# Performance work log

Measured on AMD Instinct MI355X. Metric: run time of the kernel, lower is better.

## Reference

```python
import jax, jax.numpy as jnp
import numpy as np

N = 100000   # nodes
E = 1600000  # edges
IN, H, C = 128, 128, 40


def setup_inputs() -> dict:
    key = jax.random.key(0)
    ks = jax.random.split(key, 8)
    feat = jax.random.normal(ks[0], (N, IN), jnp.float32)
    src = jax.random.randint(ks[1], (E,), 0, N, jnp.int32)
    dst = jax.random.randint(ks[2], (E,), 0, N, jnp.int32)
    # Glorot-ish init like dgl GraphConv.reset_parameters
    W0 = jax.random.normal(ks[3], (IN, H), jnp.float32) * (1.0 / np.sqrt(IN))
    W1 = jax.random.normal(ks[4], (H, H), jnp.float32) * (1.0 / np.sqrt(H))
    W2 = jax.random.normal(ks[5], (H, C), jnp.float32) * (1.0 / np.sqrt(H))
    b0 = jnp.zeros((H,), jnp.float32)
    b1 = jnp.zeros((H,), jnp.float32)
    b2 = jnp.zeros((C,), jnp.float32)
    return {"feat": feat, "src": src, "dst": dst,
            "W0": W0, "b0": b0, "W1": W1, "b1": b1, "W2": W2, "b2": b2}


def _graph_conv(h, src, dst, W, b):
    # dgl GraphConv with norm='both': D_out^{-1/2} pre-scale, sum-aggregate,
    # D_in^{-1/2} post-scale; degrees clamped to min 1. Weight applied before
    # aggregation (in_feats >= out_feats path) -- math is identical either way.
    ones = jnp.ones((src.shape[0],), h.dtype)
    deg_out = jnp.maximum(jax.ops.segment_sum(ones, src, num_segments=N), 1.0)
    deg_in = jnp.maximum(jax.ops.segment_sum(ones, dst, num_segments=N), 1.0)
    h = h * (deg_out ** -0.5)[:, None]
    h = h @ W                                   # [N, out]
    agg = jax.ops.segment_sum(h[src], dst, num_segments=N)  # gather+scatter
    return agg * (deg_in ** -0.5)[:, None] + b


def reference(feat, src, dst, W0, b0, W1, b1, W2, b2):
    h = jax.nn.relu(_graph_conv(feat, src, dst, W0, b0))  # dropout p=0 -> identity
    h = jax.nn.relu(_graph_conv(h, src, dst, W1, b1))
    return _graph_conv(h, src, dst, W2, b2)
```

## Files before the change

### kernel.cpp

```cpp
#include <hip/hip_runtime.h>

#define NN 100000
#define EE 1600000
#define ELLW 64
#define NXCD 8
#define RNG ((NN + NXCD - 1) / NXCD)
#define GEMMN ((NN + 31) / 32)
#define BUILDN ((EE / 256) * NXCD)

__device__ __forceinline__ unsigned int pack_bf2(float a, float b) {
    unsigned int ua = __float_as_uint(a);
    ua += 0x7FFFu + ((ua >> 16) & 1u);
    unsigned int ub = __float_as_uint(b);
    ub += 0x7FFFu + ((ub >> 16) & 1u);
    return (ua >> 16) | (ub & 0xFFFF0000u);
}

__device__ __forceinline__ void nt_store_f2(float* p, float x, float y) {
    unsigned long long v = (unsigned long long)__float_as_uint(x) |
                           ((unsigned long long)__float_as_uint(y) << 32);
    __builtin_nontemporal_store(v, (unsigned long long*)p);
}

__device__ __forceinline__ void gemm128_body(const float* __restrict__ X, const int* __restrict__ dout,
                                             const float* __restrict__ W, unsigned int* __restrict__ Y,
                                             int n, int row0, int tid, float* Xs, int scaled) {
    const float4* X4 = (const float4*)X;
#pragma unroll
    for (int idx = tid; idx < 1024; idx += 256) {
        int r = idx & 31, c4 = idx >> 5;
        int row = row0 + r;
        float4 v = make_float4(0.f, 0.f, 0.f, 0.f);
        float s = 0.f;
        if (row < n) {
            v = X4[(size_t)row * 32 + c4];
            s = scaled ? rsqrtf((float)max(1, dout[row])) : 1.f;
        }
        Xs[(c4 * 4 + 0) * 32 + r] = v.x * s;
        Xs[(c4 * 4 + 1) * 32 + r] = v.y * s;
        Xs[(c4 * 4 + 2) * 32 + r] = v.z * s;
        Xs[(c4 * 4 + 3) * 32 + r] = v.w * s;
    }
    __syncthreads();
    int cg = tid & 31;
    int rg = tid >> 5;
    float a[4][4];
#pragma unroll
    for (int r = 0; r < 4; ++r)
#pragma unroll
        for (int c = 0; c < 4; ++c) a[r][c] = 0.f;
    const float4* W4 = (const float4*)W;
#pragma unroll 4
    for (int k = 0; k < 128; ++k) {
        float4 xv = *(const float4*)&Xs[k * 32 + rg * 4];
        float4 wv = W4[k * 32 + cg];
        float xr[4] = {xv.x, xv.y, xv.z, xv.w};
        float wc[4] = {wv.x, wv.y, wv.z, wv.w};
#pragma unroll
        for (int r = 0; r < 4; ++r)
#pragma unroll
            for (int c = 0; c < 4; ++c) a[r][c] = fmaf(xr[r], wc[c], a[r][c]);
    }
    int rbase = row0 + rg * 4;
    uint2* Y2 = (uint2*)Y;
#pragma unroll
    for (int r = 0; r < 4; ++r) {
        if (rbase + r < n) {
            Y2[(size_t)(rbase + r) * 32 + cg] =
                make_uint2(pack_bf2(a[r][0], a[r][1]), pack_bf2(a[r][2], a[r][3]));
        }
    }
}

__global__ __launch_bounds__(256) void k_build_gemm0(const int* __restrict__ src, const int* __restrict__ dst,
                                                     int* __restrict__ din, int* __restrict__ dout,
                                                     int* __restrict__ ell,
                                                     const float* __restrict__ X, const float* __restrict__ W,
                                                     unsigned int* __restrict__ Y) {
    __shared__ float Xs[128 * 32];
    int tid = threadIdx.x;
    int q = blockIdx.x / 17, rem = blockIdx.x % 17;
    if (rem == 16) {
        gemm128_body(X, nullptr, W, Y, NN, q * 32, tid, Xs, 0);
        return;
    }
    int idx = q * 16 + rem;
    int r = idx & (NXCD - 1);
    int slice = idx >> 3;
    int i = slice * 256 + tid;
    if (i >= EE) return;
    int s = __builtin_nontemporal_load(&src[i]);
    int d = __builtin_nontemporal_load(&dst[i]);
    int lo = r * RNG, hi = lo + RNG;
    if (d >= lo && d < hi) {
        int p = atomicAdd(&din[d], 1);
        if (p < ELLW) ell[(size_t)d * ELLW + p] = s;
    }
    if (s >= lo && s < hi) {
        atomicAdd(&dout[s], 1);
    }
}

__global__ __launch_bounds__(256) void k_gemm128(const float* __restrict__ X, const int* __restrict__ dout,
                                                 const float* __restrict__ W, unsigned int* __restrict__ Y, int n) {
    __shared__ float Xs[128 * 32];
    gemm128_body(X, dout, W, Y, n, blockIdx.x * 32, threadIdx.x, Xs, 1);
}

__global__ __launch_bounds__(320) void k_gemm40(const float* __restrict__ X, const int* __restrict__ dout,
                                                const float* __restrict__ W, unsigned int* __restrict__ Y, int n) {
    __shared__ float Xs[128 * 64];
    int tid = threadIdx.x;
    int row0 = blockIdx.x * 64;
    const float4* X4 = (const float4*)X;
    for (int idx = tid; idx < 2048; idx += 320) {
        int r = idx & 63, c4 = idx >> 6;
        int row = row0 + r;
        float4 v = make_float4(0.f, 0.f, 0.f, 0.f);
        float s = 0.f;
        if (row < n) { v = X4[(size_t)row * 32 + c4]; s = rsqrtf((float)max(1, dout[row])); }
        Xs[(c4 * 4 + 0) * 64 + r] = v.x * s;
        Xs[(c4 * 4 + 1) * 64 + r] = v.y * s;
        Xs[(c4 * 4 + 2) * 64 + r] = v.z * s;
        Xs[(c4 * 4 + 3) * 64 + r] = v.w * s;
    }
    __syncthreads();
    int cg = tid % 20;
    int rg = tid / 20;
    float a0x=0,a0y=0, a1x=0,a1y=0, a2x=0,a2y=0, a3x=0,a3y=0;
    const float2* W2 = (const float2*)W;
#pragma unroll 4
    for (int k = 0; k < 128; ++k) {
        float4 xv = *(const float4*)&Xs[k * 64 + rg * 4];
        float2 wv = W2[k * 20 + cg];
        a0x += xv.x * wv.x; a0y += xv.x * wv.y;
        a1x += xv.y * wv.x; a1y += xv.y * wv.y;
        a2x += xv.z * wv.x; a2y += xv.z * wv.y;
        a3x += xv.w * wv.x; a3y += xv.w * wv.y;
    }
    int rbase = row0 + rg * 4;
    if (rbase + 0 < n) Y[(size_t)(rbase + 0) * 32 + cg] = pack_bf2(a0x, a0y);
    if (rbase + 1 < n) Y[(size_t)(rbase + 1) * 32 + cg] = pack_bf2(a1x, a1y);
    if (rbase + 2 < n) Y[(size_t)(rbase + 2) * 32 + cg] = pack_bf2(a2x, a2y);
    if (rbase + 3 < n) Y[(size_t)(rbase + 3) * 32 + cg] = pack_bf2(a3x, a3y);
}

__global__ __launch_bounds__(256) void k_gather128(const unsigned int* __restrict__ h, const int* __restrict__ din,
                                                   const int* __restrict__ dout, const int* __restrict__ ell,
                                                   const float* __restrict__ b, float* __restrict__ out,
                                                   int n, int do_relu, int so_mode) {
    int wv = threadIdx.x >> 6, lane = threadIdx.x & 63;
    int v = blockIdx.x * 4 + wv;
    if (v >= n) return;
    int dv = din[v];
    int cnt = min(dv, ELLW);
    int cl = ell[(size_t)v * ELLW + lane];
    int cls = (lane < cnt) ? cl : 0;
    float scl = 1.f;
    if (so_mode) scl = rsqrtf((float)max(1, dout[cls]));
    float sx = 0.f, sy = 0.f;
    for (int j = 0; j < cnt; j += 8) {
        int cc[8]; float mk[8]; unsigned int t[8];
#pragma unroll
        for (int k = 0; k < 8; ++k) {
            int jj = j + k;
            int jc = jj < cnt ? jj : cnt - 1;
            cc[k] = __shfl(cls, jc);
            float sw = __shfl(scl, jc);
            mk[k] = (jj < cnt) ? sw : 0.f;
        }
#pragma unroll
        for (int k = 0; k < 8; ++k)
            t[k] = h[(size_t)cc[k] * 64 + lane];
#pragma unroll
        for (int k = 0; k < 8; ++k) {
            float x = __uint_as_float(t[k] << 16);
            float y = __uint_as_float(t[k] & 0xFFFF0000u);
            sx = fmaf(mk[k], x, sx);
            sy = fmaf(mk[k], y, sy);
        }
    }
    float sc = rsqrtf((float)max(1, dv));
    float2 bb = ((const float2*)b)[lane];
    float ox = sx * sc + bb.x;
    float oy = sy * sc + bb.y;
    if (do_relu) { ox = fmaxf(ox, 0.f); oy = fmaxf(oy, 0.f); }
    nt_store_f2((float*)((float2*)out + (size_t)v * 64 + lane), ox, oy);
}

__global__ __launch_bounds__(256) void k_gather40(const unsigned short* __restrict__ h, const int* __restrict__ din,
                                                  const int* __restrict__ ell,
                                                  const float* __restrict__ b, float* __restrict__ out, int n) {
    int wv = threadIdx.x >> 6, lane = threadIdx.x & 63;
    int v = blockIdx.x * 4 + wv;
    if (v >= n) return;
    int dv = din[v];
    int cnt = min(dv, ELLW);
    int cl = ell[(size_t)v * ELLW + lane];
    int cls = (lane < cnt) ? cl : 0;
    float s = 0.f;
    for (int j = 0; j < cnt; j += 8) {
        int cc[8]; float mk[8]; unsigned short t[8];
#pragma unroll
        for (int k = 0; k < 8; ++k) {
            int jj = j + k;
            cc[k] = __shfl(cls, jj < cnt ? jj : cnt - 1);
            mk[k] = (jj < cnt) ? 1.f : 0.f;
        }
        if (lane < 40) {
#pragma unroll
            for (int k = 0; k < 8; ++k) t[k] = h[(size_t)cc[k] * 64 + lane];
#pragma unroll
            for (int k = 0; k < 8; ++k)
                s = fmaf(mk[k], __uint_as_float((unsigned int)t[k] << 16), s);
        }
    }
    if (lane < 40) {
        out[(size_t)v * 40 + lane] = s * rsqrtf((float)max(1, dv)) + b[lane];
    }
}

extern "C" void kernel_launch(void* const* d_in, const int* in_sizes, int n_in,
                              void* d_out, int out_size, void* d_ws, size_t ws_size,
                              hipStream_t stream) {
    const float* feat = (const float*)d_in[0];
    const int*   src  = (const int*)d_in[1];
    const int*   dst  = (const int*)d_in[2];
    const float* W0   = (const float*)d_in[3];
    const float* b0   = (const float*)d_in[4];
    const float* W1   = (const float*)d_in[5];
    const float* b1   = (const float*)d_in[6];
    const float* W2   = (const float*)d_in[7];
    const float* b2   = (const float*)d_in[8];
    float* out = (float*)d_out;

    char* w = (char*)d_ws;
    int*   din       = (int*)w;    w += (size_t)NN * 4;
    int*   dout      = (int*)w;    w += (size_t)NN * 4;
    int*   ell       = (int*)w;    w += (size_t)NN * ELLW * 4;
    unsigned int* h2 = (unsigned int*)w; w += (size_t)NN * 128 * 2;
    unsigned int* h40 = (unsigned int*)w; w += (size_t)NN * 32 * 4;
    float* agg       = (float*)w;  w += (size_t)NN * 128 * 4;

    hipMemsetAsync(d_ws, 0, (size_t)NN * 8, stream);

    int gath_grid = (NN + 3) / 4;

    k_build_gemm0<<<GEMMN * 17, 256, 0, stream>>>(src, dst, din, dout, ell, feat, W0, h2);
    k_gather128<<<gath_grid, 256, 0, stream>>>(h2, din, dout, ell, b0, agg, NN, 1, 1);
    k_gemm128<<<GEMMN, 256, 0, stream>>>(agg, dout, W1, h2, NN);
    k_gather128<<<gath_grid, 256, 0, stream>>>(h2, din, dout, ell, b1, agg, NN, 1, 0);
    k_gemm40<<<(NN + 63) / 64, 320, 0, stream>>>(agg, dout, W2, h40, NN);
    k_gather40<<<gath_grid, 256, 0, stream>>>((const unsigned short*)h40, din, ell, b2, out, NN);
}
```

Measured before the change: 567.0 us.

## Phase-partition gather by source-id range for L2 locality; unfuse build and first GEMM

Replaces the one-node-per-wave 128-wide gather with a kernel where each wave owns 13 destination nodes. It walks 13 phases, and in each phase gathers only neighbours whose source id falls in one 8192-node range (selected by ballot), so the rows being read from the bf16 feature table are meant to stay resident in L2. The first layer's out-degree pre-scale moves from the gather into the GEMM, which now runs as a separate kernel after a standalone graph-build kernel instead of being fused with it. In exchange, gathers are issued one neighbour at a time instead of 8-wide batches, which weakens memory-level parallelism. Splitting the fused build/GEMM launch also gives up the overlap between the atomic-heavy build and the GEMM.

```diff
diff --git a/kernel.cpp b/kernel.cpp
--- a/kernel.cpp
+++ b/kernel.cpp
@@ -7,6 +7,9 @@
 #define RNG ((NN + NXCD - 1) / NXCD)
 #define GEMMN ((NN + 31) / 32)
 #define BUILDN ((EE / 256) * NXCD)
+#define GBLK 2048
+#define NPW 13
+#define NPH 13
 
 __device__ __forceinline__ unsigned int pack_bf2(float a, float b) {
     unsigned int ua = __float_as_uint(a);
@@ -22,9 +25,30 @@
     __builtin_nontemporal_store(v, (unsigned long long*)p);
 }
 
-__device__ __forceinline__ void gemm128_body(const float* __restrict__ X, const int* __restrict__ dout,
-                                             const float* __restrict__ W, unsigned int* __restrict__ Y,
-                                             int n, int row0, int tid, float* Xs, int scaled) {
+__global__ __launch_bounds__(256) void k_build(const int* __restrict__ src, const int* __restrict__ dst,
+                                               int* __restrict__ din, int* __restrict__ dout,
+                                               int* __restrict__ ell, int e) {
+    int r = blockIdx.x & (NXCD - 1);
+    int slice = blockIdx.x >> 3;
+    int i = slice * 256 + threadIdx.x;
+    if (i >= e) return;
+    int s = __builtin_nontemporal_load(&src[i]);
+    int d = __builtin_nontemporal_load(&dst[i]);
+    int lo = r * RNG, hi = lo + RNG;
+    if (d >= lo && d < hi) {
+        int p = atomicAdd(&din[d], 1);
+        if (p < ELLW) ell[(size_t)d * ELLW + p] = s;
+    }
+    if (s >= lo && s < hi) {
+        atomicAdd(&dout[s], 1);
+    }
+}
+
+__global__ __launch_bounds__(256) void k_gemm128(const float* __restrict__ X, const int* __restrict__ deg,
+                                                 const float* __restrict__ W, unsigned int* __restrict__ Y, int n) {
+    __shared__ float Xs[128 * 32];
+    int tid = threadIdx.x;
+    int row0 = blockIdx.x * 32;
     const float4* X4 = (const float4*)X;
 #pragma unroll
     for (int idx = tid; idx < 1024; idx += 256) {
@@ -34,7 +58,7 @@
         float s = 0.f;
         if (row < n) {
             v = X4[(size_t)row * 32 + c4];
-            s = scaled ? rsqrtf((float)max(1, dout[row])) : 1.f;
+            s = rsqrtf((float)max(1, deg[row]));
         }
         Xs[(c4 * 4 + 0) * 32 + r] = v.x * s;
         Xs[(c4 * 4 + 1) * 32 + r] = v.y * s;
@@ -72,42 +96,7 @@
     }
 }
 
-__global__ __launch_bounds__(256) void k_build_gemm0(const int* __restrict__ src, const int* __restrict__ dst,
-                                                     int* __restrict__ din, int* __restrict__ dout,
-                                                     int* __restrict__ ell,
-                                                     const float* __restrict__ X, const float* __restrict__ W,
-                                                     unsigned int* __restrict__ Y) {
-    __shared__ float Xs[128 * 32];
-    int tid = threadIdx.x;
-    int q = blockIdx.x / 17, rem = blockIdx.x % 17;
-    if (rem == 16) {
-        gemm128_body(X, nullptr, W, Y, NN, q * 32, tid, Xs, 0);
-        return;
-    }
-    int idx = q * 16 + rem;
-    int r = idx & (NXCD - 1);
-    int slice = idx >> 3;
-    int i = slice * 256 + tid;
-    if (i >= EE) return;
-    int s = __builtin_nontemporal_load(&src[i]);
-    int d = __builtin_nontemporal_load(&dst[i]);
-    int lo = r * RNG, hi = lo + RNG;
-    if (d >= lo && d < hi) {
-        int p = atomicAdd(&din[d], 1);
-        if (p < ELLW) ell[(size_t)d * ELLW + p] = s;
-    }
-    if (s >= lo && s < hi) {
-        atomicAdd(&dout[s], 1);
-    }
-}
-
-__global__ __launch_bounds__(256) void k_gemm128(const float* __restrict__ X, const int* __restrict__ dout,
-                                                 const float* __restrict__ W, unsigned int* __restrict__ Y, int n) {
-    __shared__ float Xs[128 * 32];
-    gemm128_body(X, dout, W, Y, n, blockIdx.x * 32, threadIdx.x, Xs, 1);
-}
-
-__global__ __launch_bounds__(320) void k_gemm40(const float* __restrict__ X, const int* __restrict__ dout,
+__global__ __launch_bounds__(320) void k_gemm40(const float* __restrict__ X, const int* __restrict__ deg,
                                                 const float* __restrict__ W, unsigned int* __restrict__ Y, int n) {
     __shared__ float Xs[128 * 64];
     int tid = threadIdx.x;
@@ -118,7 +107,7 @@
         int row = row0 + r;
         float4 v = make_float4(0.f, 0.f, 0.f, 0.f);
         float s = 0.f;
-        if (row < n) { v = X4[(size_t)row * 32 + c4]; s = rsqrtf((float)max(1, dout[row])); }
+        if (row < n) { v = X4[(size_t)row * 32 + c4]; s = rsqrtf((float)max(1, deg[row])); }
         Xs[(c4 * 4 + 0) * 64 + r] = v.x * s;
         Xs[(c4 * 4 + 1) * 64 + r] = v.y * s;
         Xs[(c4 * 4 + 2) * 64 + r] = v.z * s;
@@ -145,47 +134,53 @@
     if (rbase + 3 < n) Y[(size_t)(rbase + 3) * 32 + cg] = pack_bf2(a3x, a3y);
 }
 
-__global__ __launch_bounds__(256) void k_gather128(const unsigned int* __restrict__ h, const int* __restrict__ din,
-                                                   const int* __restrict__ dout, const int* __restrict__ ell,
-                                                   const float* __restrict__ b, float* __restrict__ out,
-                                                   int n, int do_relu, int so_mode) {
-    int wv = threadIdx.x >> 6, lane = threadIdx.x & 63;
-    int v = blockIdx.x * 4 + wv;
-    if (v >= n) return;
-    int dv = din[v];
-    int cnt = min(dv, ELLW);
-    int cl = ell[(size_t)v * ELLW + lane];
-    int cls = (lane < cnt) ? cl : 0;
-    float scl = 1.f;
-    if (so_mode) scl = rsqrtf((float)max(1, dout[cls]));
-    float sx = 0.f, sy = 0.f;
-    for (int j = 0; j < cnt; j += 8) {
-        int cc[8]; float mk[8]; unsigned int t[8];
-#pragma unroll
-        for (int k = 0; k < 8; ++k) {
-            int jj = j + k;
-            int jc = jj < cnt ? jj : cnt - 1;
-            cc[k] = __shfl(cls, jc);
-            float sw = __shfl(scl, jc);
-            mk[k] = (jj < cnt) ? sw : 0.f;
-        }
-#pragma unroll
-        for (int k = 0; k < 8; ++k)
-            t[k] = h[(size_t)cc[k] * 64 + lane];
-#pragma unroll
-        for (int k = 0; k < 8; ++k) {
-            float x = __uint_as_float(t[k] << 16);
-            float y = __uint_as_float(t[k] & 0xFFFF0000u);
-            sx = fmaf(mk[k], x, sx);
-            sy = fmaf(mk[k], y, sy);
-        }
-    }
-    float sc = rsqrtf((float)max(1, dv));
+__global__ __launch_bounds__(256) void k_gather128p(const unsigned int* __restrict__ h,
+                                                    const int* __restrict__ din, const int* __restrict__ ell,
+                                                    const float* __restrict__ b, float* __restrict__ out,
+                                                    int do_relu) {
+    int lane = threadIdx.x & 63;
+    int gw = (blockIdx.x * 256 + threadIdx.x) >> 6;
+    int v0 = gw * NPW;
+    float sx[NPW], sy[NPW];
+    int cls[NPW];
+    int cnt[NPW];
+#pragma unroll
+    for (int i = 0; i < NPW; ++i) {
+        sx[i] = 0.f; sy[i] = 0.f; cnt[i] = 0; cls[i] = 0x7FFFFFFF;
+        int v = v0 + i;
+        if (v < NN) {
+            int dv = din[v];
+            cnt[i] = dv;
+            int e = ell[(size_t)v * ELLW + lane];
+            if (lane < dv) cls[i] = e;
+        }
+    }
+    for (int p = 0; p < NPH; ++p) {
+#pragma unroll
+        for (int i = 0; i < NPW; ++i) {
+            unsigned long long m = __ballot(((unsigned int)cls[i] >> 13) == (unsigned int)p);
+            while (m) {
+                int j = __builtin_ctzll(m);
+                m &= m - 1;
+                int c = __shfl(cls[i], j);
+                unsigned int t = h[(size_t)c * 64 + lane];
+                sx[i] += __uint_as_float(t << 16);
+                sy[i] += __uint_as_float(t & 0xFFFF0000u);
+            }
+        }
+    }
     float2 bb = ((const float2*)b)[lane];
-    float ox = sx * sc + bb.x;
-    float oy = sy * sc + bb.y;
-    if (do_relu) { ox = fmaxf(ox, 0.f); oy = fmaxf(oy, 0.f); }
-    nt_store_f2((float*)((float2*)out + (size_t)v * 64 + lane), ox, oy);
+#pragma unroll
+    for (int i = 0; i < NPW; ++i) {
+        int v = v0 + i;
+        if (v < NN) {
+            float sc = rsqrtf((float)max(1, cnt[i]));
+            float ox = sx[i] * sc + bb.x;
+            float oy = sy[i] * sc + bb.y;
+            if (do_relu) { ox = fmaxf(ox, 0.f); oy = fmaxf(oy, 0.f); }
+            nt_store_f2((float*)((float2*)out + (size_t)v * 64 + lane), ox, oy);
+        }
+    }
 }
 
 __global__ __launch_bounds__(256) void k_gather40(const unsigned short* __restrict__ h, const int* __restrict__ din,
@@ -246,10 +241,11 @@
 
     int gath_grid = (NN + 3) / 4;
 
-    k_build_gemm0<<<GEMMN * 17, 256, 0, stream>>>(src, dst, din, dout, ell, feat, W0, h2);
-    k_gather128<<<gath_grid, 256, 0, stream>>>(h2, din, dout, ell, b0, agg, NN, 1, 1);
+    k_build<<<BUILDN, 256, 0, stream>>>(src, dst, din, dout, ell, EE);
+    k_gemm128<<<GEMMN, 256, 0, stream>>>(feat, dout, W0, h2, NN);
+    k_gather128p<<<GBLK, 256, 0, stream>>>(h2, din, ell, b0, agg, 1);
     k_gemm128<<<GEMMN, 256, 0, stream>>>(agg, dout, W1, h2, NN);
-    k_gather128<<<gath_grid, 256, 0, stream>>>(h2, din, dout, ell, b1, agg, NN, 1, 0);
+    k_gather128p<<<GBLK, 256, 0, stream>>>(h2, din, ell, b1, agg, 1);
     k_gemm40<<<(NN + 63) / 64, 320, 0, stream>>>(agg, dout, W2, h40, NN);
     k_gather40<<<gath_grid, 256, 0, stream>>>((const unsigned short*)h40, din, ell, b2, out, NN);
 }
```

Measured after the change: 791.0 us. 39.5% more time.
